# Performance work log

Hardware: AMD Instinct MI355X
Metric: run time of the kernel (lower is better)

## Reference

```python
import jax, jax.numpy as jnp
import numpy as np


def _rope(x, pos, theta):
    # x: [b, s, h, d], pos: [s] int. Standard interleaved RoPE on even/odd pairs.
    d = x.shape[-1]
    inv_freq = theta ** (-jnp.arange(0, d, 2, dtype=jnp.float32) / d)  # [d/2]
    ang = pos.astype(jnp.float32)[:, None] * inv_freq                  # [s, d/2]
    cos = jnp.cos(ang)[None, :, None, :]
    sin = jnp.sin(ang)[None, :, None, :]
    x1 = x[..., 0::2]
    x2 = x[..., 1::2]
    rot = jnp.stack([x1 * cos - x2 * sin, x1 * sin + x2 * cos], axis=-1)
    return rot.reshape(x.shape)


def setup_inputs() -> dict:
    key = jax.random.key(0)
    ks = jax.random.split(key, 5)
    b, s, d = 4, 2048, 1024
    scale = 1.0 / np.sqrt(d)
    return {
        "x": jax.random.normal(ks[0], (b, s, d), dtype=jnp.float32),
        "W_Q": jax.random.normal(ks[1], (d, d), dtype=jnp.float32) * scale,
        "W_K": jax.random.normal(ks[2], (d, d), dtype=jnp.float32) * scale,
        "W_V": jax.random.normal(ks[3], (d, d), dtype=jnp.float32) * scale,
        "W_O": jax.random.normal(ks[4], (d, d), dtype=jnp.float32) * scale,
        "token_positions": jnp.arange(s, dtype=jnp.int32),
    }


def reference(x, W_Q, W_K, W_V, W_O, token_positions):
    num_heads = 16
    theta = 10000.0
    b, s, d_model = x.shape
    d_k = d_model // num_heads

    Q = x @ W_Q.T  # [b, s, d_model]
    K = x @ W_K.T
    V = x @ W_V.T

    # split heads: last dim is [h0 | h1 | ...] so reshape to [b, s, h, d_k]
    Qh = Q.reshape(b, s, num_heads, d_k)
    Kh = K.reshape(b, s, num_heads, d_k)
    Vh = V.reshape(b, s, num_heads, d_k)

    Qh = _rope(Qh, token_positions, theta)
    Kh = _rope(Kh, token_positions, theta)

    scores = jnp.einsum("bqhd,bkhd->bhqk", Qh, Kh) / jnp.sqrt(
        jnp.asarray(d_k, dtype=x.dtype)
    )
    causal = jnp.tril(jnp.ones((s, s), dtype=bool))  # True = keep
    scores = jnp.where(causal[None, None, :, :], scores, jnp.asarray(-jnp.inf, x.dtype))
    probs = jax.nn.softmax(scores, axis=-1)

    out = jnp.einsum("bhqk,bkhd->bqhd", probs, Vh).reshape(b, s, d_model)
    return out @ W_O.T
```

## Files before the change

kernel.cpp:

```cpp
#include <hip/hip_runtime.h>
#include <hip/hip_bf16.h>
#include <type_traits>

typedef __attribute__((ext_vector_type(8))) short short8;
typedef __attribute__((ext_vector_type(4))) short s16x4;
typedef __attribute__((ext_vector_type(4))) float f32x4;
typedef unsigned short u16;
typedef unsigned int   u32;
typedef unsigned long long u64;


#if __has_builtin(__builtin_amdgcn_mfma_f32_16x16x16bf16_1k)
#define MFMA16(a, b, c) __builtin_amdgcn_mfma_f32_16x16x16bf16_1k(a, b, c, 0, 0, 0)
#define HAVE_MFMA16 1
#elif __has_builtin(__builtin_amdgcn_mfma_f32_16x16x16_bf16)
#define MFMA16(a, b, c) __builtin_amdgcn_mfma_f32_16x16x16_bf16(a, b, c, 0, 0, 0)
#define HAVE_MFMA16 1
#else
#define HAVE_MFMA16 0
#endif

static __device__ __forceinline__ u16 f2b(float f) {
  u32 u = __builtin_bit_cast(u32, f);
  u = (u + 0x7fffu + ((u >> 16) & 1u)) >> 16;
  return (u16)u;
}
static __device__ __forceinline__ float b2f(u16 h) {
  return __builtin_bit_cast(float, ((u32)h) << 16);
}
static __device__ __forceinline__ u32 pkbf(float a, float b) {
  union { __hip_bfloat162 t; u32 u; } c;
  c.t = __float22bfloat162_rn(make_float2(a, b));
  return c.u;
}

typedef __attribute__((address_space(1))) const unsigned int gas_u32;
typedef __attribute__((address_space(3))) unsigned int las_u32;
static __device__ __forceinline__ void glds16(const u16* g, u16* l) {
  __builtin_amdgcn_global_load_lds((gas_u32*)g, (las_u32*)l, 16, 0, 0);
}

__global__ __launch_bounds__(256) void cvt_all(
    const float* __restrict__ x, const float* __restrict__ wq,
    const float* __restrict__ wk, const float* __restrict__ wv,
    const float* __restrict__ wo, u16* __restrict__ xb, u16* __restrict__ wqb,
    u16* __restrict__ wkb, u16* __restrict__ wvb, u16* __restrict__ wob) {
  int u = blockIdx.x * 256 + threadIdx.x;
  if (u >= 3145728) return;
  const float* src; u16* dst; int off;
  if (u < 2097152) { src = x; dst = xb; off = u; }
  else {
    int t = u - 2097152;
    int w = t >> 18;
    off = t & 0x3FFFF;
    src = (w == 0) ? wq : (w == 1) ? wk : (w == 2) ? wv : wo;
    dst = (w == 0) ? wqb : (w == 1) ? wkb : (w == 2) ? wvb : wob;
  }
  int i = off * 4;
  float4 v = *(const float4*)(src + i);
  union { u16 us[4]; u64 ull; } o;
  o.us[0] = f2b(v.x); o.us[1] = f2b(v.y); o.us[2] = f2b(v.z); o.us[3] = f2b(v.w);
  *(u64*)(dst + i) = o.ull;
}

template <typename OT, int TM>
static __device__ __forceinline__ void gemm_body(const u16* __restrict__ A,
                                                 const u16* __restrict__ B,
                                                 OT* __restrict__ C,
                                                 int m0, int n0) {
  __shared__ u16 As[4096];
  __shared__ u16 Bs[4096];

  const int tid  = threadIdx.x;
  const int lane = tid & 63;
  const int wv   = tid >> 6;
  const int quad = lane >> 4;
  const int cc   = lane & 15;
  const int wr   = wv >> 1;
  const int wc   = wv & 1;

  f32x4 acc[4][4];
#pragma unroll
  for (int i = 0; i < 4; i++)
#pragma unroll
    for (int j = 0; j < 4; j++) acc[i][j] = (f32x4){0.f, 0.f, 0.f, 0.f};

  const int p0 = wv * 128 + lane;
  const int p1 = p0 + 64;
  const int r0 = p0 >> 2, g0 = (p0 & 3) ^ (r0 & 3);
  const int r1 = p1 >> 2, g1 = (p1 & 3) ^ (r1 & 3);
  const u16* gA0 = A + (size_t)(m0 + r0) * 1024 + g0 * 8;
  const u16* gA1 = A + (size_t)(m0 + r1) * 1024 + g1 * 8;
  const u16* gB0 = B + (size_t)(n0 + r0) * 1024 + g0 * 8;
  const u16* gB1 = B + (size_t)(n0 + r1) * 1024 + g1 * 8;
  u16* lA = As + wv * 1024;
  u16* lB = Bs + wv * 1024;

  for (int k0 = 0; k0 < 1024; k0 += 32) {
    __syncthreads();
    glds16(gA0 + k0, lA);
    glds16(gA1 + k0, lA + 512);
    glds16(gB0 + k0, lB);
    glds16(gB1 + k0, lB + 512);
    __syncthreads();

    short8 af[4], bf[4];
#pragma unroll
    for (int mt = 0; mt < 4; mt++) {
      int ra = wr * 64 + mt * 16 + cc;
      af[mt] = *(const short8*)&As[ra * 32 + ((quad ^ (ra & 3)) * 8)];
    }
#pragma unroll
    for (int nt = 0; nt < 4; nt++) {
      int rb = wc * 64 + nt * 16 + cc;
      bf[nt] = *(const short8*)&Bs[rb * 32 + ((quad ^ (rb & 3)) * 8)];
    }
#pragma unroll
    for (int mt = 0; mt < 4; mt++)
#pragma unroll
      for (int nt = 0; nt < 4; nt++)
        acc[mt][nt] = __builtin_amdgcn_mfma_f32_16x16x32_bf16(af[mt], bf[nt], acc[mt][nt], 0, 0, 0);
  }

#pragma unroll
  for (int mt = 0; mt < 4; mt++)
#pragma unroll
    for (int nt = 0; nt < 4; nt++) {
      if constexpr (TM == 2) {
        const int col = n0 + wc * 64 + nt * 16 + cc;
        const int rowbase = m0 + wr * 64 + mt * 16 + quad * 4;
        const int bsel = rowbase >> 11;
        const int s0 = rowbase & 2047;
        union { u16 us[4]; u64 ull; } o;
#pragma unroll
        for (int r = 0; r < 4; r++) o.us[r] = f2b(acc[mt][nt][r]);
        *(u64*)&C[((size_t)(bsel * 1024 + col)) * 2048 + s0] = o.ull;
      } else {
#pragma unroll
        for (int r = 0; r < 4; r++) {
          int row = m0 + wr * 64 + mt * 16 + quad * 4 + r;
          int col = n0 + wc * 64 + nt * 16 + cc;
          if constexpr (TM == 0)
            C[(size_t)row * 1024 + col] = acc[mt][nt][r];
          else
            C[(size_t)row * 1024 + col] = f2b(acc[mt][nt][r]);
        }
      }
    }
}

__global__ __launch_bounds__(256) void gemm_qkv(const u16* __restrict__ A,
                                                const u16* __restrict__ Bq,
                                                const u16* __restrict__ Bk,
                                                const u16* __restrict__ Bv,
                                                u16* __restrict__ Q,
                                                u16* __restrict__ K,
                                                u16* __restrict__ Vt) {
  int sel = blockIdx.x >> 3;
  int m0 = blockIdx.y * 128, n0 = (blockIdx.x & 7) * 128;
  if (sel == 0)      gemm_body<u16, 1>(A, Bq, Q,  m0, n0);
  else if (sel == 1) gemm_body<u16, 1>(A, Bk, K,  m0, n0);
  else               gemm_body<u16, 2>(A, Bv, Vt, m0, n0);
}

__global__ __launch_bounds__(256) void gemm_out(const u16* __restrict__ A,
                                                const u16* __restrict__ B,
                                                float* __restrict__ C) {
  gemm_body<float, 0>(A, B, C, blockIdx.y * 128, blockIdx.x * 128);
}

__global__ __launch_bounds__(256) void rope_kernel(u16* __restrict__ Q,
                                                   u16* __restrict__ K,
                                                   const int* __restrict__ pos) {
  u16* T = blockIdx.y ? K : Q;
  const float sc = blockIdx.y ? 1.0f : 0.18033688011112042f;
  int idx = blockIdx.x * 256 + threadIdx.x;
  int row = idx >> 9;
  int p   = idx & 511;
  int i   = p & 31;
  int col = (p >> 5) * 64 + 2 * i;
  int s   = row & 2047;
  float ps  = (float)pos[s];
  float inv = exp2f(-(float)i * 0.41524101186092033f);
  float ang = ps * inv;
  float sn, cs;
  sincosf(ang, &sn, &cs);
  u32 v = *(u32*)(T + (size_t)row * 1024 + col);
  float x1 = b2f((u16)(v & 0xffffu));
  float x2 = b2f((u16)(v >> 16));
  float y1 = (x1 * cs - x2 * sn) * sc;
  float y2 = (x1 * sn + x2 * cs) * sc;
  *(u32*)(T + (size_t)row * 1024 + col) = (u32)f2b(y1) | ((u32)f2b(y2) << 16);
}


#define S_STEP(MT, SV)                                                     \
  do {                                                                     \
    __builtin_amdgcn_s_setprio(1);                                         \
    _Pragma("unroll")                                                      \
    for (int nt = 0; nt < 8; ++nt) {                                       \
      const int rbase = (nt * 16 + cc) * 64;                               \
      short8 bk0 = *(const short8*)&Ks[cur][rbase + pk0];                  \
      short8 bk1 = *(const short8*)&Ks[cur][rbase + (pk0 ^ 32)];           \
      f32x4 z = (f32x4){0.f, 0.f, 0.f, 0.f};                               \
      z = __builtin_amdgcn_mfma_f32_16x16x32_bf16(bk0, qf[MT][0], z, 0, 0, 0); \
      SV[nt] = __builtin_amdgcn_mfma_f32_16x16x32_bf16(bk1, qf[MT][1], z, 0, 0, 0); \
    }                                                                      \
    __builtin_amdgcn_s_setprio(0);                                         \
  } while (0)

#define MASK_STEP(MT, SV)                                                  \
  do {                                                                     \
    const int qg = q0 + wv * 32 + MT * 16 + cc;                            \
    const int kb = kt * 128 + quad * 4;                                    \
    _Pragma("unroll")                                                      \
    for (int nt = 0; nt < 8; ++nt)                                         \
      _Pragma("unroll")                                                    \
      for (int r = 0; r < 4; ++r)                                          \
        if (kb + nt * 16 + r > qg) SV[nt][r] = -3.0e38f;                   \
  } while (0)

#define MAXRED_STEP(MT, SV)                                                \
  do {                                                                     \
    float mx = fmaxf(fmaxf(SV[0][0], SV[0][1]), fmaxf(SV[0][2], SV[0][3]));\
    _Pragma("unroll")                                                      \
    for (int nt = 1; nt < 8; ++nt)                                         \
      mx = fmaxf(mx, fmaxf(fmaxf(SV[nt][0], SV[nt][1]),                    \
                           fmaxf(SV[nt][2], SV[nt][3])));                  \
    mx = fmaxf(mx, __shfl_xor(mx, 16));                                    \
    mx = fmaxf(mx, __shfl_xor(mx, 32));                                    \
    if (!__all(mx <= m_i[MT] + 11.0f)) {                                   \
      const float mn = fmaxf(m_i[MT], mx);                                 \
      const float al = exp2f(m_i[MT] - mn);                                \
      m_i[MT] = mn;                                                        \
      l_i[MT] *= al;                                                       \
      f32x4 al4;                                                           \
      _Pragma("unroll")                                                    \
      for (int r = 0; r < 4; ++r) al4[r] = __shfl(al, quad * 4 + r);       \
      _Pragma("unroll")                                                    \
      for (int nt = 0; nt < 4; ++nt) o_acc[MT][nt] *= al4;                 \
    }                                                                      \
  } while (0)

#if HAVE_MFMA16
#define EXPPV_STEP(MT, SV)                                                 \
  do {                                                                     \
    const float mu = m_i[MT];                                              \
    float ps = 0.f;                                                        \
    __builtin_amdgcn_s_setprio(1);                                         \
    _Pragma("unroll")                                                      \
    for (int kk = 0; kk < 8; ++kk) {                                       \
      float e0 = exp2f(SV[kk][0] - mu);                                    \
      float e1 = exp2f(SV[kk][1] - mu);                                    \
      float e2 = exp2f(SV[kk][2] - mu);                                    \
      float e3 = exp2f(SV[kk][3] - mu);                                    \
      ps += (e0 + e1) + (e2 + e3);                                         \
      union { u32 w[2]; s16x4 v; } pu;                                     \
      pu.w[0] = pkbf(e0, e1);                                              \
      pu.w[1] = pkbf(e2, e3);                                              \
      const int pos = (kk * 2 + (quad >> 1) + cc) & 15;                    \
      _Pragma("unroll")                                                    \
      for (int nt = 0; nt < 4; ++nt) {                                     \
        s16x4 bv = *(const s16x4*)&Vs[(nt * 16 + cc) * 128 + pos * 8 + (quad & 1) * 4]; \
        o_acc[MT][nt] = MFMA16(pu.v, bv, o_acc[MT][nt]);                   \
      }                                                                    \
    }                                                                      \
    __builtin_amdgcn_s_setprio(0);                                         \
    l_i[MT] += ps;                                                         \
  } while (0)
#else
#define EXPPV_STEP(MT, SV)                                                 \
  do {                                                                     \
    const float mu = m_i[MT];                                              \
    float ps = 0.f;                                                        \
    s16x4 pf[8];                                                           \
    _Pragma("unroll")                                                      \
    for (int nt = 0; nt < 8; ++nt) {                                       \
      float e0 = exp2f(SV[nt][0] - mu);                                    \
      float e1 = exp2f(SV[nt][1] - mu);                                    \
      float e2 = exp2f(SV[nt][2] - mu);                                    \
      float e3 = exp2f(SV[nt][3] - mu);                                    \
      ps += (e0 + e1) + (e2 + e3);                                         \
      union { u32 w[2]; s16x4 v; } pu;                                     \
      pu.w[0] = pkbf(e0, e1);                                              \
      pu.w[1] = pkbf(e2, e3);                                              \
      pf[nt] = pu.v;                                                       \
    }                                                                      \
    l_i[MT] += ps;                                                         \
    _Pragma("unroll")                                                      \
    for (int nt = 0; nt < 8; ++nt) {                                       \
      union { s16x4 v; u64 ull; } pu2; pu2.v = pf[nt];                     \
      *(u64*)&Ps[(wv * 16 + cc) * 136 + nt * 16 + quad * 4] = pu2.ull;     \
    }                                                                      \
    short8 pa[4];                                                          \
    _Pragma("unroll")                                                      \
    for (int ks = 0; ks < 4; ++ks)                                         \
      pa[ks] = *(const short8*)&Ps[(wv * 16 + cc) * 136 + ks * 32 + quad * 8];\
    _Pragma("unroll")                                                      \
    for (int nt = 0; nt < 4; ++nt) {                                       \
      const int rv = (nt * 16 + cc) * 128;                                 \
      _Pragma("unroll")                                                    \
      for (int ks = 0; ks < 4; ++ks) {                                     \
        const int pos = (ks * 4 + quad + cc) & 15;                         \
        short8 bv = *(const short8*)&Vs[rv + pos * 8];                     \
        o_acc[MT][nt] = __builtin_amdgcn_mfma_f32_16x16x32_bf16(pa[ks], bv, o_acc[MT][nt], 0, 0, 0); \
      }                                                                    \
    }                                                                      \
  } while (0)
#endif

__global__ __launch_bounds__(256, 3) void attn_kernel(const u16* __restrict__ Q,
                                                      const u16* __restrict__ K,
                                                      const u16* __restrict__ Vt,
                                                      u16* __restrict__ O) {
  __shared__ u16 Ks[2][8192];
  __shared__ u16 Vs[8192];
#if !HAVE_MFMA16
  __shared__ u16 Ps[4 * 16 * 136];
#endif

  const int bh = blockIdx.x;
  const int qt = 15 - blockIdx.y;
  const int b = bh >> 4, h = bh & 15;
  const int tid  = threadIdx.x;
  const int lane = tid & 63;
  const int wv   = tid >> 6;
  const int quad = lane >> 4;
  const int cc   = lane & 15;
  const int q0   = qt * 128;

  short8 qf[2][2];
#pragma unroll
  for (int mt = 0; mt < 2; mt++) {
    const u16* qp = Q + (size_t)(b * 2048 + q0 + wv * 32 + mt * 16 + cc) * 1024 + h * 64;
    qf[mt][0] = *(const short8*)(qp + quad * 8);
    qf[mt][1] = *(const short8*)(qp + 32 + quad * 8);
  }

  f32x4 o_acc[2][4];
  float m_i[2] = {-3.0e38f, -3.0e38f}, l_i[2] = {0.f, 0.f};
#pragma unroll
  for (int mt = 0; mt < 2; mt++)
#pragma unroll
    for (int nt = 0; nt < 4; nt++) o_acc[mt][nt] = (f32x4){0.f, 0.f, 0.f, 0.f};

  const u16* Kp = K + ((size_t)(b * 2048) + wv * 32 + (lane >> 3)) * 1024 + h * 64 +
                  (((lane & 7) ^ (lane >> 3)) * 8);
  const u16* Vp[4];
#pragma unroll
  for (int j = 0; j < 4; j++) {
    int rl = wv * 16 + j * 4 + (lane >> 4);
    int g  = ((lane & 15) - rl) & 15;
    Vp[j] = Vt + ((size_t)(bh * 64) + rl) * 2048 + g * 8;
  }

  const int nkt = qt + 1;
  const int pk0 = (quad ^ (cc & 7)) * 8;

#pragma unroll
  for (int j = 0; j < 4; j++)
    glds16(Kp + j * 8192, &Ks[0][wv * 2048 + j * 512]);
  __syncthreads();

  for (int kt = 0; kt < nkt; ++kt) {
    const int cur = kt & 1;

#pragma unroll
    for (int j = 0; j < 4; j++)
      glds16(Vp[j] + kt * 128, Vs + wv * 2048 + j * 512);
    if (kt + 1 < nkt) {
#pragma unroll
      for (int j = 0; j < 4; j++)
        glds16(Kp + (size_t)(kt + 1) * 131072 + j * 8192,
               &Ks[cur ^ 1][wv * 2048 + j * 512]);
    }

    const bool diag = (kt == qt);

    {
      f32x4 s[8];
      S_STEP(0, s);
      if (diag) MASK_STEP(0, s);
      MAXRED_STEP(0, s);

      __syncthreads();

      EXPPV_STEP(0, s);
    }

    {
      f32x4 s[8];
      S_STEP(1, s);
      if (diag) MASK_STEP(1, s);
      MAXRED_STEP(1, s);
      EXPPV_STEP(1, s);
    }

    __syncthreads();
  }

#pragma unroll
  for (int mt = 0; mt < 2; ++mt) {
    float l = l_i[mt];
    l += __shfl_xor(l, 16);
    l += __shfl_xor(l, 32);
    const float linv = 1.0f / l;
    f32x4 li4;
#pragma unroll
    for (int r = 0; r < 4; ++r) li4[r] = __shfl(linv, quad * 4 + r);
    const int rowb = b * 2048 + q0 + wv * 32 + mt * 16 + quad * 4;
#pragma unroll
    for (int nt = 0; nt < 4; ++nt)
#pragma unroll
      for (int r = 0; r < 4; ++r)
        O[(size_t)(rowb + r) * 1024 + h * 64 + nt * 16 + cc] = f2b(o_acc[mt][nt][r] * li4[r]);
  }
}

extern "C" void kernel_launch(void* const* d_in, const int* in_sizes, int n_in,
                              void* d_out, int out_size, void* d_ws, size_t ws_size,
                              hipStream_t stream) {
  const float* x  = (const float*)d_in[0];
  const float* wq = (const float*)d_in[1];
  const float* wk = (const float*)d_in[2];
  const float* wv = (const float*)d_in[3];
  const float* wo = (const float*)d_in[4];
  const int* pos  = (const int*)d_in[5];
  float* out = (float*)d_out;

  char* ws = (char*)d_ws;
  u16* xb  = (u16*)(ws);
  u16* aO  = (u16*)(ws);
  u16* wqb = (u16*)(ws + (16ull << 20));
  u16* wkb = (u16*)(ws + (18ull << 20));
  u16* wvb = (u16*)(ws + (20ull << 20));
  u16* wob = (u16*)(ws + (22ull << 20));
  u16* Qb  = (u16*)(ws + (24ull << 20));
  u16* Kb  = (u16*)(ws + (40ull << 20));
  u16* vt  = (u16*)(ws + (56ull << 20));

  cvt_all<<<12288, 256, 0, stream>>>(x, wq, wk, wv, wo, xb, wqb, wkb, wvb, wob);
  gemm_qkv<<<dim3(24, 64), 256, 0, stream>>>(xb, wqb, wkb, wvb, Qb, Kb, vt);
  rope_kernel<<<dim3(16384, 2), 256, 0, stream>>>(Qb, Kb, pos);
  attn_kernel<<<dim3(64, 16), 256, 0, stream>>>(Qb, Kb, vt, aO);
  gemm_out<<<dim3(8, 64), 256, 0, stream>>>(aO, wob, out);
}
```

Before: 287.9 us.

## Fuse RoPE into QKV GEMM epilogue and swizzle GEMM block order

```diff
diff --git a/kernel.cpp b/kernel.cpp
--- a/kernel.cpp
+++ b/kernel.cpp
@@ -67,7 +67,9 @@
 static __device__ __forceinline__ void gemm_body(const u16* __restrict__ A,
                                                  const u16* __restrict__ B,
                                                  OT* __restrict__ C,
-                                                 int m0, int n0) {
+                                                 int m0, int n0,
+                                                 const int* __restrict__ pos,
+                                                 float rsc) {
   __shared__ u16 As[4096];
   __shared__ u16 Bs[4096];
 
@@ -122,31 +124,56 @@
         acc[mt][nt] = __builtin_amdgcn_mfma_f32_16x16x32_bf16(af[mt], bf[nt], acc[mt][nt], 0, 0, 0);
   }
 
-#pragma unroll
-  for (int mt = 0; mt < 4; mt++)
-#pragma unroll
-    for (int nt = 0; nt < 4; nt++) {
-      if constexpr (TM == 2) {
+  if constexpr (TM == 3) {
+    float prow[4][4];
+#pragma unroll
+    for (int mt = 0; mt < 4; mt++)
+#pragma unroll
+      for (int r = 0; r < 4; r++)
+        prow[mt][r] = (float)pos[(m0 + wr * 64 + mt * 16 + quad * 4 + r) & 2047];
+#pragma unroll
+    for (int mt = 0; mt < 4; mt++)
+#pragma unroll
+      for (int nt = 0; nt < 4; nt++) {
         const int col = n0 + wc * 64 + nt * 16 + cc;
-        const int rowbase = m0 + wr * 64 + mt * 16 + quad * 4;
-        const int bsel = rowbase >> 11;
-        const int s0 = rowbase & 2047;
-        union { u16 us[4]; u64 ull; } o;
-#pragma unroll
-        for (int r = 0; r < 4; r++) o.us[r] = f2b(acc[mt][nt][r]);
-        *(u64*)&C[((size_t)(bsel * 1024 + col)) * 2048 + s0] = o.ull;
-      } else {
+        const int fi  = (col & 63) >> 1;
+        const float inv = exp2f(-(float)fi * 0.41524101186092033f);
+        const bool odd = col & 1;
 #pragma unroll
         for (int r = 0; r < 4; r++) {
-          int row = m0 + wr * 64 + mt * 16 + quad * 4 + r;
-          int col = n0 + wc * 64 + nt * 16 + cc;
-          if constexpr (TM == 0)
-            C[(size_t)row * 1024 + col] = acc[mt][nt][r];
-          else
-            C[(size_t)row * 1024 + col] = f2b(acc[mt][nt][r]);
+          const int row = m0 + wr * 64 + mt * 16 + quad * 4 + r;
+          float sn, cs;
+          sincosf(prow[mt][r] * inv, &sn, &cs);
+          const float x = acc[mt][nt][r];
+          const float p = __shfl_xor(x, 1);
+          const float y = odd ? (p * sn + x * cs) : (x * cs - p * sn);
+          C[(size_t)row * 1024 + col] = f2b(y * rsc);
         }
       }
-    }
+  } else {
+#pragma unroll
+    for (int mt = 0; mt < 4; mt++)
+#pragma unroll
+      for (int nt = 0; nt < 4; nt++) {
+        if constexpr (TM == 2) {
+          const int col = n0 + wc * 64 + nt * 16 + cc;
+          const int rowbase = m0 + wr * 64 + mt * 16 + quad * 4;
+          const int bsel = rowbase >> 11;
+          const int s0 = rowbase & 2047;
+          union { u16 us[4]; u64 ull; } o;
+#pragma unroll
+          for (int r = 0; r < 4; r++) o.us[r] = f2b(acc[mt][nt][r]);
+          *(u64*)&C[((size_t)(bsel * 1024 + col)) * 2048 + s0] = o.ull;
+        } else {
+#pragma unroll
+          for (int r = 0; r < 4; r++) {
+            int row = m0 + wr * 64 + mt * 16 + quad * 4 + r;
+            int col = n0 + wc * 64 + nt * 16 + cc;
+            C[(size_t)row * 1024 + col] = acc[mt][nt][r];
+          }
+        }
+      }
+  }
 }
 
 __global__ __launch_bounds__(256) void gemm_qkv(const u16* __restrict__ A,
@@ -155,42 +182,25 @@
                                                 const u16* __restrict__ Bv,
                                                 u16* __restrict__ Q,
                                                 u16* __restrict__ K,
-                                                u16* __restrict__ Vt) {
-  int sel = blockIdx.x >> 3;
-  int m0 = blockIdx.y * 128, n0 = (blockIdx.x & 7) * 128;
-  if (sel == 0)      gemm_body<u16, 1>(A, Bq, Q,  m0, n0);
-  else if (sel == 1) gemm_body<u16, 1>(A, Bk, K,  m0, n0);
-  else               gemm_body<u16, 2>(A, Bv, Vt, m0, n0);
+                                                u16* __restrict__ Vt,
+                                                const int* __restrict__ pos) {
+  const int lin = blockIdx.x;
+  const int swz = (lin & 7) * 192 + (lin >> 3);
+  const int m0  = (swz / 24) * 128;
+  const int rem = swz % 24;
+  const int sel = rem >> 3;
+  const int n0  = (rem & 7) * 128;
+  if (sel == 0)      gemm_body<u16, 3>(A, Bq, Q,  m0, n0, pos, 0.18033688011112042f);
+  else if (sel == 1) gemm_body<u16, 3>(A, Bk, K,  m0, n0, pos, 1.0f);
+  else               gemm_body<u16, 2>(A, Bv, Vt, m0, n0, nullptr, 0.f);
 }
 
 __global__ __launch_bounds__(256) void gemm_out(const u16* __restrict__ A,
                                                 const u16* __restrict__ B,
                                                 float* __restrict__ C) {
-  gemm_body<float, 0>(A, B, C, blockIdx.y * 128, blockIdx.x * 128);
-}
-
-__global__ __launch_bounds__(256) void rope_kernel(u16* __restrict__ Q,
-                                                   u16* __restrict__ K,
-                                                   const int* __restrict__ pos) {
-  u16* T = blockIdx.y ? K : Q;
-  const float sc = blockIdx.y ? 1.0f : 0.18033688011112042f;
-  int idx = blockIdx.x * 256 + threadIdx.x;
-  int row = idx >> 9;
-  int p   = idx & 511;
-  int i   = p & 31;
-  int col = (p >> 5) * 64 + 2 * i;
-  int s   = row & 2047;
-  float ps  = (float)pos[s];
-  float inv = exp2f(-(float)i * 0.41524101186092033f);
-  float ang = ps * inv;
-  float sn, cs;
-  sincosf(ang, &sn, &cs);
-  u32 v = *(u32*)(T + (size_t)row * 1024 + col);
-  float x1 = b2f((u16)(v & 0xffffu));
-  float x2 = b2f((u16)(v >> 16));
-  float y1 = (x1 * cs - x2 * sn) * sc;
-  float y2 = (x1 * sn + x2 * cs) * sc;
-  *(u32*)(T + (size_t)row * 1024 + col) = (u32)f2b(y1) | ((u32)f2b(y2) << 16);
+  const int lin = blockIdx.x;
+  const int swz = (lin & 7) * 64 + (lin >> 3);
+  gemm_body<float, 0>(A, B, C, (swz >> 3) * 128, (swz & 7) * 128, nullptr, 0.f);
 }
 
 
@@ -440,8 +450,7 @@
   u16* vt  = (u16*)(ws + (56ull << 20));
 
   cvt_all<<<12288, 256, 0, stream>>>(x, wq, wk, wv, wo, xb, wqb, wkb, wvb, wob);
-  gemm_qkv<<<dim3(24, 64), 256, 0, stream>>>(xb, wqb, wkb, wvb, Qb, Kb, vt);
-  rope_kernel<<<dim3(16384, 2), 256, 0, stream>>>(Qb, Kb, pos);
+  gemm_qkv<<<1536, 256, 0, stream>>>(xb, wqb, wkb, wvb, Qb, Kb, vt, pos);
   attn_kernel<<<dim3(64, 16), 256, 0, stream>>>(Qb, Kb, vt, aO);
-  gemm_out<<<dim3(8, 64), 256, 0, stream>>>(aO, wob, out);
-}
+  gemm_out<<<512, 256, 0, stream>>>(aO, wob, out);
+}
```

After: 653.7 us. 2.27x slower.
